# Kernel tuning notes

Hardware: AMD Instinct MI355X
Metric: run time of the kernel (lower is better)

Reference implementation:

```python
import jax, jax.numpy as jnp
import numpy as np

B, T, L, DC, DW, H, V = 128, 256, 4, 128, 128, 256, 6000
NEG = -1e30

def _lstm(x, c, h, kernel, bias):
    # TF BasicLSTMCell, forget_bias=0, gate order i, j, f, o
    z = jnp.concatenate([x, h], axis=-1) @ kernel + bias
    i, j, f, o = jnp.split(z, 4, axis=-1)
    nc = c * jax.nn.sigmoid(f) + jax.nn.sigmoid(i) * jnp.tanh(j)
    nh = jnp.tanh(nc) * jax.nn.sigmoid(o)
    return nc, nh

def _forward(chars, char_emb, reset_W, reset_b, com_W, com_b, lstm_kernel, lstm_bias, pred_W, pred_b, score_U, bos):
    Bn, Tn = chars.shape
    dt = char_emb.dtype
    # init agenda entry: BoS vector through LSTM from zero state
    c0 = jnp.zeros((Bn, H), dt)
    h0 = jnp.zeros((Bn, H), dt)
    x0 = jnp.broadcast_to(bos, (Bn, DW))
    c1, h1 = _lstm(x0, c0, h0, lstm_kernel, lstm_bias)
    pred0 = jnp.tanh(h1 @ pred_W + pred_b)
    # rolling buffer over the last L agenda entries (slot w-1 = position t-w)
    buf_pred = jnp.repeat(pred0[:, None, :], L, axis=1)
    buf_c = jnp.repeat(c1[:, None, :], L, axis=1)
    buf_h = jnp.repeat(h1[:, None, :], L, axis=1)
    # windows[t, b, j] = char at position t-j (age j), front-padded
    padded = jnp.pad(chars, ((0, 0), (L - 1, 0)))
    gi = jnp.arange(Tn)[:, None] + (L - 1) - jnp.arange(L)[None, :]
    windows = jnp.transpose(padded[:, gi], (1, 0, 2))  # [T, B, L]
    wlens = jnp.arange(1, L + 1)
    cmask = (jnp.arange(L)[None, :] < wlens[:, None]).astype(dt)  # [W, C]
    inv_len = (1.0 / wlens).astype(dt)

    def step(carry, xs):
        buf_pred, buf_c, buf_h = carry
        window, t = xs
        emb = char_emb[window]  # [B, L, DC] (ages 0..L-1)
        # per-wlen reset gate (separate weights per word length)
        g = jax.nn.sigmoid(jnp.einsum('bcd,wde->bwce', emb, reset_W) + reset_b[None, :, None, :])
        proj = jnp.tanh(jnp.einsum('bwcd,de->bwce', g * emb[:, None], com_W) + com_b)  # [B,W,C,DW]
        word = jnp.einsum('bwce,wc->bwe', proj, cmask) * inv_len[None, :, None]  # [B,W,DW] mean over the wlen chars
        score = jnp.sum((buf_pred + score_U) * word, axis=-1)  # [B,W] local score vs prev prediction
        score = jnp.where((wlens <= t + 1)[None, :], score, NEG)
        best = jnp.argmax(score, axis=1)  # greedy choice of word length
        b3 = best[:, None, None]
        word_b = jnp.take_along_axis(word, b3, axis=1)[:, 0]
        c_prev = jnp.take_along_axis(buf_c, b3, axis=1)[:, 0]
        h_prev = jnp.take_along_axis(buf_h, b3, axis=1)[:, 0]
        nc, nh = _lstm(word_b, c_prev, h_prev, lstm_kernel, lstm_bias)
        npred = jnp.tanh(nh @ pred_W + pred_b)
        carry = (jnp.concatenate([npred[:, None], buf_pred[:, :-1]], axis=1),
                 jnp.concatenate([nc[:, None], buf_c[:, :-1]], axis=1),
                 jnp.concatenate([nh[:, None], buf_h[:, :-1]], axis=1))
        best_score = jnp.take_along_axis(score, best[:, None], axis=1)[:, 0]
        return carry, (best_score, best + 1)

    _, (scores, wl) = jax.lax.scan(step, (buf_pred, buf_c, buf_h), (windows, jnp.arange(Tn)))
    return scores.T, wl.T  # [B,T] best local score, [B,T] chosen word length

def setup_inputs() -> dict:
    key = jax.random.key(0)
    ks = jax.random.split(key, 12)
    f = lambda k, s: 0.1 * jax.random.normal(k, s, dtype=jnp.float32)
    return {
        'chars': jax.random.randint(ks[0], (B, T), 0, V, dtype=jnp.int32),
        'char_emb': f(ks[1], (V, DC)),
        'reset_W': f(ks[2], (L, DC, DC)),
        'reset_b': f(ks[3], (L, DC)),
        'com_W': f(ks[4], (DC, DW)),
        'com_b': f(ks[5], (DW,)),
        'lstm_kernel': f(ks[6], (DW + H, 4 * H)),
        'lstm_bias': jnp.zeros((4 * H,), jnp.float32),
        'pred_W': f(ks[7], (H, DW)),
        'pred_b': f(ks[8], (DW,)),
        'score_U': f(ks[9], (DW,)),
        'bos': f(ks[10], (DW,)),
    }

def reference(chars, char_emb, reset_W, reset_b, com_W, com_b, lstm_kernel, lstm_bias, pred_W, pred_b, score_U, bos):
    return _forward(chars, char_emb, reset_W, reset_b, com_W, com_b, lstm_kernel, lstm_bias, pred_W, pred_b, score_U, bos)
```

## Files before the change

### kernel.cpp

```cpp
#include <hip/hip_runtime.h>

#define B_ 128
#define T_ 256
#define L_ 4
#define DC_ 128
#define DW_ 128
#define H_ 256
#define V_ 6000
#define Z4_ 1024
#define S_ 4
#define R_ 2
#define G_ 64
#define NEGF -1e30f

#define WS_VTAB  4096
#define WS_NH    (WS_VTAB + V_*L_*DW_*4)
#define WS_PP    (WS_NH + (size_t)2*G_*R_*H_*8)

typedef unsigned long long u64w;

__device__ __forceinline__ float sigm(float x) { return 1.0f / (1.0f + expf(-x)); }
__device__ __forceinline__ void pub64(u64w* p, float v, unsigned stamp) {
  u64w w = ((u64w)__float_as_uint(v) << 32) | (u64w)stamp;
  __hip_atomic_store(p, w, __ATOMIC_RELAXED, __HIP_MEMORY_SCOPE_AGENT);
}
__device__ __forceinline__ u64w ld64(const u64w* p) {
  return __hip_atomic_load(p, __ATOMIC_RELAXED, __HIP_MEMORY_SCOPE_AGENT);
}
__device__ __forceinline__ float hi32(u64w w) {
  return __uint_as_float((unsigned)(w >> 32));
}
__device__ __forceinline__ float bcast(float v, int l) {
  return __int_as_float(__builtin_amdgcn_readlane(__float_as_int(v), l));
}
__device__ __forceinline__ int amax4(const float* sc) {
  float bs = sc[0]; int bw = 0;
  if (sc[1] > bs) { bs = sc[1]; bw = 1; }
  if (sc[2] > bs) { bs = sc[2]; bw = 2; }
  if (sc[3] > bs) { bs = sc[3]; bw = 3; }
  return bw;
}
__device__ __forceinline__ float invlen(int w) {
  return (w == 0) ? 1.0f : (w == 1) ? 0.5f : (w == 2) ? (1.0f / 3.0f) : 0.25f;
}

__global__ __launch_bounds__(512) void vtab_kernel(
    const float* __restrict__ char_emb, const float* __restrict__ reset_W,
    const float* __restrict__ reset_b, const float* __restrict__ com_W,
    const float* __restrict__ com_b, float* __restrict__ Vtab)
{
  const int v = blockIdx.x;
  const int tid = threadIdx.x;
  const int w = tid >> 7;
  const int e = tid & 127;
  __shared__ float emb[DC_];
  __shared__ float ge[L_][DC_];
  if (tid < DC_) emb[tid] = char_emb[v * DC_ + tid];
  __syncthreads();
  float acc = reset_b[w * DC_ + e];
  const float* W = reset_W + (size_t)w * DC_ * DC_;
  #pragma unroll 8
  for (int k = 0; k < DC_; ++k) acc = fmaf(emb[k], W[k * DC_ + e], acc);
  ge[w][e] = sigm(acc) * emb[e];
  __syncthreads();
  float acc2 = com_b[e];
  #pragma unroll 8
  for (int k = 0; k < DC_; ++k) acc2 = fmaf(ge[w][k], com_W[k * DW_ + e], acc2);
  Vtab[((size_t)v * L_ + w) * DW_ + e] = tanhf(acc2);
}

__global__ __launch_bounds__(512, 2) void seq_kernel(
    const int* __restrict__ chars, const float* __restrict__ Vtab,
    const float* __restrict__ Kmat, const float* __restrict__ lstm_bias,
    const float* __restrict__ pred_W, const float* __restrict__ pred_b,
    const float* __restrict__ score_U, const float* __restrict__ bos,
    float* __restrict__ out, u64w* __restrict__ nh_mb, u64w* __restrict__ pp_mb)
{
  const int blk = blockIdx.x;
  const int s = blk >> 6;
  const int g = blk & 63;
  const int tid = threadIdx.x;
  const int lane = tid & 63;
  const int wv = tid >> 6;
  const int c = tid & 255;
  const int koff = (tid < 256) ? 0 : 192;
  const int colg = (c >> 6) * H_ + s * 64 + (c & 63);
  const int row0 = g * R_;

  float wreg[192];
  #pragma unroll
  for (int i = 0; i < 192; ++i)
    wreg[i] = Kmat[(size_t)(koff + i) * Z4_ + colg];

  __shared__ float ringVt[R_][4][512];
  __shared__ float pring[4][R_][DW_];
  __shared__ float zring[4][R_][256];
  __shared__ float cring[4][R_][64];
  __shared__ float zhA[R_][256];
  __shared__ float zhB[R_][256];
  __shared__ float zxL[R_][256];
  __shared__ float predWL[64][128];
  __shared__ float h1tmp[H_];
  __shared__ int   charsL[R_][T_];
  __shared__ float biasC[256], UL[128], pbL[128];
  __shared__ float scL[R_][L_];

  if (tid < 256) biasC[tid] = lstm_bias[(tid >> 6) * H_ + s * 64 + (tid & 63)];
  if (tid < 128) { UL[tid] = score_U[tid]; pbL[tid] = pred_b[tid]; }
  for (int i = tid; i < 64 * 128; i += 512)
    predWL[i >> 7][i & 127] = pred_W[(size_t)(s * 64 + (i >> 7)) * DW_ + (i & 127)];
  for (int i = tid; i < R_ * T_; i += 512)
    charsL[i >> 8][i & 255] = chars[(row0 + (i >> 8)) * T_ + (i & 255)];
  for (int i = tid; i < R_ * 4 * 512; i += 512) ((float*)ringVt)[i] = 0.0f;
  __syncthreads();

  {
    float* zb = &zring[0][0][0];
    for (int c2 = tid; c2 < Z4_; c2 += 512) {
      float a = lstm_bias[c2];
      #pragma unroll 8
      for (int k = 0; k < DC_; ++k) a = fmaf(bos[k], Kmat[(size_t)k * Z4_ + c2], a);
      zb[c2] = a;
    }
    __syncthreads();
    if (tid < H_) {
      float zi = zb[tid], zj = zb[H_ + tid], zo = zb[3 * H_ + tid];
      float nc = sigm(zi) * tanhf(zj);
      float nh = tanhf(nc) * sigm(zo);
      h1tmp[tid] = nh;
      int hl = tid - s * 64;
      if (hl >= 0 && hl < 64) {
        #pragma unroll
        for (int q = 0; q < 4; ++q)
          #pragma unroll
          for (int r = 0; r < R_; ++r) cring[q][r][hl] = nc;
      }
    }
    __syncthreads();
    {
      int kq = tid >> 7, e = tid & 127;
      float a = 0.0f;
      #pragma unroll 8
      for (int k = kq * 64; k < kq * 64 + 64; ++k)
        a = fmaf(h1tmp[k], pred_W[(size_t)k * DW_ + e], a);
      ((float*)zhA)[kq * 128 + e] = a;
    }
    __syncthreads();
    if (tid < 128) {
      const float* pa = (const float*)zhA;
      float p = tanhf(pbL[tid] + pa[tid] + pa[128 + tid] + pa[256 + tid] + pa[384 + tid]);
      #pragma unroll
      for (int q = 0; q < 4; ++q)
        #pragma unroll
        for (int r = 0; r < R_; ++r) pring[q][r][tid] = p;
    }
    __syncthreads();
    {
      float a = 0.0f;
      if (tid < 256) {
        #pragma unroll
        for (int k = 0; k < 64; ++k) a = fmaf(h1tmp[k], wreg[128 + k], a);
      } else {
        #pragma unroll
        for (int k = 0; k < 192; ++k) a = fmaf(h1tmp[64 + k], wreg[k], a);
      }
      __syncthreads();
      if (tid < 256) zhA[0][c] = a; else zhB[0][c] = a;
    }
    __syncthreads();
    if (tid < 256) {
      float z1 = zhA[0][tid] + zhB[0][tid];
      #pragma unroll
      for (int q = 0; q < 4; ++q)
        #pragma unroll
        for (int r = 0; r < R_; ++r) zring[q][r][tid] = z1;
    }
    __syncthreads();
  }

  for (int t = 0; t < T_; ++t) {
    const int slot = t & 3;
    const int parR = (t - 1) & 1;
    const int parW = t & 1;
    const unsigned stR = (unsigned)t;
    const unsigned stW = (unsigned)(t + 1);

    if ((wv >> 1) == 1) {
      int i2 = tid & 127;
      #pragma unroll
      for (int r = 0; r < R_; ++r) {
        const float* vp = Vtab + (size_t)charsL[r][t] * 512;
        #pragma unroll
        for (int q = 0; q < 4; ++q) ringVt[r][slot][q * 128 + i2] = vp[q * 128 + i2];
      }
    }

    if (t > 0) {
      const u64w* nb = nh_mb + ((size_t)parR * G_ + g) * (R_ * H_);
      if (wv < 2) {
        const u64w* ppb = pp_mb + ((size_t)parR * G_ + g) * (S_ * R_ * 128) + wv * 128;
        u64w pw0[S_], pw1[S_], nw0, nw1;
        for (;;) {
          #pragma unroll
          for (int sp = 0; sp < S_; ++sp) {
            pw0[sp] = ld64(ppb + (size_t)sp * (R_ * 128) + lane);
            pw1[sp] = ld64(ppb + (size_t)sp * (R_ * 128) + lane + 64);
          }
          nw0 = ld64(nb + lane);
          nw1 = ld64(nb + H_ + lane);
          int ok = ((unsigned)nw0 == stR) & ((unsigned)nw1 == stR);
          #pragma unroll
          for (int sp = 0; sp < S_; ++sp)
            ok &= ((unsigned)pw0[sp] == stR) & ((unsigned)pw1[sp] == stR);
          if (__all(ok)) break;
          __builtin_amdgcn_s_sleep(1);
        }
        float a0 = pbL[lane], a1 = pbL[lane + 64];
        #pragma unroll
        for (int sp = 0; sp < S_; ++sp) {
          a0 += hi32(pw0[sp]);
          a1 += hi32(pw1[sp]);
        }
        int ps = (t - 1) & 3;
        pring[ps][wv][lane] = tanhf(a0);
        pring[ps][wv][lane + 64] = tanhf(a1);
        float nv0 = hi32(nw0), nv1 = hi32(nw1);
        float z0 = 0.0f, z1 = 0.0f;
        #pragma unroll
        for (int k = 0; k < 64; ++k) {
          float w = wreg[128 + k];
          z0 = fmaf(bcast(nv0, k), w, z0);
          z1 = fmaf(bcast(nv1, k), w, z1);
        }
        zhA[0][c] = z0; zhA[1][c] = z1;
      } else if (wv < 4) {
        u64w nw0, nw1;
        for (;;) {
          nw0 = ld64(nb + lane);
          nw1 = ld64(nb + H_ + lane);
          int ok = ((unsigned)nw0 == stR) & ((unsigned)nw1 == stR);
          if (__all(ok)) break;
          __builtin_amdgcn_s_sleep(1);
        }
        float nv0 = hi32(nw0), nv1 = hi32(nw1);
        float z0 = 0.0f, z1 = 0.0f;
        #pragma unroll
        for (int k = 0; k < 64; ++k) {
          float w = wreg[128 + k];
          z0 = fmaf(bcast(nv0, k), w, z0);
          z1 = fmaf(bcast(nv1, k), w, z1);
        }
        zhA[0][c] = z0; zhA[1][c] = z1;
      } else {
        u64w nw[2][3];
        for (;;) {
          #pragma unroll
          for (int r = 0; r < 2; ++r)
            #pragma unroll
            for (int j = 0; j < 3; ++j)
              nw[r][j] = ld64(nb + (size_t)r * H_ + 64 + j * 64 + lane);
          int ok = 1;
          #pragma unroll
          for (int r = 0; r < 2; ++r)
            #pragma unroll
            for (int j = 0; j < 3; ++j)
              ok &= ((unsigned)nw[r][j] == stR);
          if (__all(ok)) break;
          __builtin_amdgcn_s_sleep(1);
        }
        float a0 = 0.0f, a1 = 0.0f;
        #pragma unroll
        for (int j = 0; j < 3; ++j) {
          float nv0 = hi32(nw[0][j]), nv1 = hi32(nw[1][j]);
          #pragma unroll
          for (int k = 0; k < 64; ++k) {
            float w = wreg[j * 64 + k];
            a0 = fmaf(bcast(nv0, k), w, a0);
            a1 = fmaf(bcast(nv1, k), w, a1);
          }
        }
        zhB[0][c] = a0; zhB[1][c] = a1;
      }
    }
    __syncthreads();

    if (t > 0) {
      int r = tid >> 8, cc = tid & 255;
      zring[(t - 1) & 3][r][cc] = zhA[r][cc] + zhB[r][cc];
    }
    {
      int r = wv >> 2, w = wv & 3;
      int ps = (t - 1 - w) & 3;
      float il = invlen(w);
      float acc = 0.0f;
      #pragma unroll
      for (int hf = 0; hf < 2; ++hf) {
        int e = lane + hf * 64;
        float sa = 0.0f;
        #pragma unroll
        for (int c2 = 0; c2 < L_; ++c2)
          if (c2 <= w) sa += ringVt[r][(t - c2) & 3][w * 128 + e];
        acc = fmaf(pring[ps][r][e] + UL[e], sa * il, acc);
      }
      #pragma unroll
      for (int off = 32; off; off >>= 1) acc += __shfl_down(acc, off);
      if (lane == 0) scL[r][w] = (w <= t) ? acc : NEGF;
    }
    __syncthreads();

    if (tid < 256) {
      float vt0[2], vt1[2];
      #pragma unroll
      for (int r = 0; r < 2; ++r) {
        int bw = amax4(scL[r]);
        float il = invlen(bw);
        float v0 = 0.f, v1 = 0.f;
        #pragma unroll
        for (int c2 = 0; c2 < L_; ++c2)
          if (c2 <= bw) {
            v0 += ringVt[r][(t - c2) & 3][bw * 128 + lane];
            v1 += ringVt[r][(t - c2) & 3][bw * 128 + 64 + lane];
          }
        vt0[r] = v0 * il; vt1[r] = v1 * il;
      }
      float a0 = 0.f, a1 = 0.f;
      #pragma unroll
      for (int k = 0; k < 64; ++k) {
        float w0 = wreg[k], w1 = wreg[64 + k];
        a0 = fmaf(bcast(vt0[0], k), w0, a0);
        a1 = fmaf(bcast(vt0[1], k), w0, a1);
        a0 = fmaf(bcast(vt1[0], k), w1, a0);
        a1 = fmaf(bcast(vt1[1], k), w1, a1);
      }
      zxL[0][c] = a0; zxL[1][c] = a1;
      if (s == 0 && tid < R_) {
        int bw = amax4(scL[tid]);
        out[(row0 + tid) * T_ + t] = scL[tid][bw];
        out[B_ * T_ + (row0 + tid) * T_ + t] = (float)(bw + 1);
      }
    }
    __syncthreads();

    if (tid < 128) {
      int r = wv, hl = lane;
      int bw = amax4(scL[r]);
      int zs = (t - 1 - bw) & 3;
      float zg[4];
      #pragma unroll
      for (int gi = 0; gi < 4; ++gi) {
        int cc = gi * 64 + hl;
        zg[gi] = biasC[cc] + zring[zs][r][cc] + zxL[r][cc];
      }
      float cp = cring[zs][r][hl];
      float nc = cp * sigm(zg[2]) + sigm(zg[0]) * tanhf(zg[1]);
      float nh = tanhf(nc) * sigm(zg[3]);
      cring[slot][r][hl] = nc;
      pub64(&nh_mb[((size_t)parW * G_ + g) * (R_ * H_) + (size_t)r * H_ + s * 64 + hl],
            nh, stW);
      float p0 = 0.f, p1 = 0.f;
      #pragma unroll
      for (int kk = 0; kk < 64; ++kk) {
        float nb2 = __shfl(nh, kk, 64);
        p0 = fmaf(nb2, predWL[kk][lane], p0);
        p1 = fmaf(nb2, predWL[kk][lane + 64], p1);
      }
      u64w* pb = pp_mb + ((size_t)parW * G_ + g) * (S_ * R_ * 128)
               + (size_t)s * (R_ * 128) + (size_t)r * 128;
      pub64(pb + lane, p0, stW);
      pub64(pb + lane + 64, p1, stW);
    }
  }
}

extern "C" void kernel_launch(void* const* d_in, const int* in_sizes, int n_in,
                              void* d_out, int out_size, void* d_ws, size_t ws_size,
                              hipStream_t stream) {
  const int*   chars     = (const int*)d_in[0];
  const float* char_emb  = (const float*)d_in[1];
  const float* reset_W   = (const float*)d_in[2];
  const float* reset_b   = (const float*)d_in[3];
  const float* com_W     = (const float*)d_in[4];
  const float* com_b     = (const float*)d_in[5];
  const float* lstm_k    = (const float*)d_in[6];
  const float* lstm_bias = (const float*)d_in[7];
  const float* pred_W    = (const float*)d_in[8];
  const float* pred_b    = (const float*)d_in[9];
  const float* score_U   = (const float*)d_in[10];
  const float* bos       = (const float*)d_in[11];

  char* ws = (char*)d_ws;
  float* Vtab = (float*)(ws + WS_VTAB);
  u64w* nh_mb = (u64w*)(ws + WS_NH);
  u64w* pp_mb = (u64w*)(ws + WS_PP);

  vtab_kernel<<<V_, 512, 0, stream>>>(char_emb, reset_W, reset_b, com_W, com_b, Vtab);
  seq_kernel<<<256, 512, 0, stream>>>(chars, Vtab, lstm_k, lstm_bias, pred_W,
                                      pred_b, score_U, bos, (float*)d_out,
                                      nh_mb, pp_mb);
}
```

Before: 2.275 ms.

## Rebalance per-step work across waves and raise priority on critical path

Restructures the per-timestep schedule. Waves 0-3 now compute the word scores for both rows, then their 64-wide recurrent h-projection. Waves 4-7 split their 192-wide h-projection, running one third in the score phase and the remaining two thirds alongside the zx projection, and write zring directly, which removes the zhB buffer and one combine pass. It also raises wave priority (s_setprio) around the prediction reduction and the LSTM/publish section that other blocks wait on, and replaces __shfl with bcast. The aim is to balance work across waves and shorten the cross-block critical path, at the cost of more register pressure from the held mailbox values.

```diff
diff --git a/kernel.cpp b/kernel.cpp
--- a/kernel.cpp
+++ b/kernel.cpp
@@ -97,7 +97,6 @@
   __shared__ float zring[4][R_][256];
   __shared__ float cring[4][R_][64];
   __shared__ float zhA[R_][256];
-  __shared__ float zhB[R_][256];
   __shared__ float zxL[R_][256];
   __shared__ float predWL[64][128];
   __shared__ float h1tmp[H_];
@@ -165,11 +164,11 @@
         for (int k = 0; k < 192; ++k) a = fmaf(h1tmp[64 + k], wreg[k], a);
       }
       __syncthreads();
-      if (tid < 256) zhA[0][c] = a; else zhB[0][c] = a;
+      if (tid < 256) ((float*)zhA)[c] = a; else ((float*)zhA)[256 + c] = a;
     }
     __syncthreads();
     if (tid < 256) {
-      float z1 = zhA[0][tid] + zhB[0][tid];
+      float z1 = ((float*)zhA)[tid] + ((float*)zhA)[256 + tid];
       #pragma unroll
       for (int q = 0; q < 4; ++q)
         #pragma unroll
@@ -184,6 +183,11 @@
     const int parW = t & 1;
     const unsigned stR = (unsigned)t;
     const unsigned stW = (unsigned)(t + 1);
+    const u64w* nb = nh_mb + ((size_t)parR * G_ + g) * (R_ * H_);
+
+    u64w nwreg0, nwreg1;
+    u64w nwU[2][3];
+    float zh0 = 0.0f, zh1 = 0.0f;
 
     if ((wv >> 1) == 1) {
       int i2 = tid & 127;
@@ -196,7 +200,6 @@
     }
 
     if (t > 0) {
-      const u64w* nb = nh_mb + ((size_t)parR * G_ + g) * (R_ * H_);
       if (wv < 2) {
         const u64w* ppb = pp_mb + ((size_t)parR * G_ + g) * (S_ * R_ * 128) + wv * 128;
         u64w pw0[S_], pw1[S_], nw0, nw1;
@@ -215,6 +218,7 @@
           if (__all(ok)) break;
           __builtin_amdgcn_s_sleep(1);
         }
+        __builtin_amdgcn_s_setprio(1);
         float a0 = pbL[lane], a1 = pbL[lane + 64];
         #pragma unroll
         for (int sp = 0; sp < S_; ++sp) {
@@ -224,15 +228,8 @@
         int ps = (t - 1) & 3;
         pring[ps][wv][lane] = tanhf(a0);
         pring[ps][wv][lane + 64] = tanhf(a1);
-        float nv0 = hi32(nw0), nv1 = hi32(nw1);
-        float z0 = 0.0f, z1 = 0.0f;
-        #pragma unroll
-        for (int k = 0; k < 64; ++k) {
-          float w = wreg[128 + k];
-          z0 = fmaf(bcast(nv0, k), w, z0);
-          z1 = fmaf(bcast(nv1, k), w, z1);
-        }
-        zhA[0][c] = z0; zhA[1][c] = z1;
+        __builtin_amdgcn_s_setprio(0);
+        nwreg0 = nw0; nwreg1 = nw1;
       } else if (wv < 4) {
         u64w nw0, nw1;
         for (;;) {
@@ -242,69 +239,66 @@
           if (__all(ok)) break;
           __builtin_amdgcn_s_sleep(1);
         }
-        float nv0 = hi32(nw0), nv1 = hi32(nw1);
-        float z0 = 0.0f, z1 = 0.0f;
-        #pragma unroll
-        for (int k = 0; k < 64; ++k) {
-          float w = wreg[128 + k];
-          z0 = fmaf(bcast(nv0, k), w, z0);
-          z1 = fmaf(bcast(nv1, k), w, z1);
-        }
-        zhA[0][c] = z0; zhA[1][c] = z1;
+        nwreg0 = nw0; nwreg1 = nw1;
       } else {
-        u64w nw[2][3];
         for (;;) {
           #pragma unroll
           for (int r = 0; r < 2; ++r)
             #pragma unroll
             for (int j = 0; j < 3; ++j)
-              nw[r][j] = ld64(nb + (size_t)r * H_ + 64 + j * 64 + lane);
+              nwU[r][j] = ld64(nb + (size_t)r * H_ + 64 + j * 64 + lane);
           int ok = 1;
           #pragma unroll
           for (int r = 0; r < 2; ++r)
             #pragma unroll
             for (int j = 0; j < 3; ++j)
-              ok &= ((unsigned)nw[r][j] == stR);
+              ok &= ((unsigned)nwU[r][j] == stR);
           if (__all(ok)) break;
           __builtin_amdgcn_s_sleep(1);
         }
+      }
+    }
+    __syncthreads();
+
+    if (wv < 4) {
+      #pragma unroll
+      for (int r = 0; r < 2; ++r) {
+        int w = wv;
+        int ps = (t - 1 - w) & 3;
+        float il = invlen(w);
+        float acc = 0.0f;
+        #pragma unroll
+        for (int hf = 0; hf < 2; ++hf) {
+          int e = lane + hf * 64;
+          float sa = 0.0f;
+          #pragma unroll
+          for (int c2 = 0; c2 < L_; ++c2)
+            if (c2 <= w) sa += ringVt[r][(t - c2) & 3][w * 128 + e];
+          acc = fmaf(pring[ps][r][e] + UL[e], sa * il, acc);
+        }
+        #pragma unroll
+        for (int off = 32; off; off >>= 1) acc += __shfl_down(acc, off);
+        if (lane == 0) scL[r][w] = (w <= t) ? acc : NEGF;
+      }
+      if (t > 0) {
+        float nv0 = hi32(nwreg0), nv1 = hi32(nwreg1);
         float a0 = 0.0f, a1 = 0.0f;
         #pragma unroll
-        for (int j = 0; j < 3; ++j) {
-          float nv0 = hi32(nw[0][j]), nv1 = hi32(nw[1][j]);
-          #pragma unroll
-          for (int k = 0; k < 64; ++k) {
-            float w = wreg[j * 64 + k];
-            a0 = fmaf(bcast(nv0, k), w, a0);
-            a1 = fmaf(bcast(nv1, k), w, a1);
-          }
-        }
-        zhB[0][c] = a0; zhB[1][c] = a1;
-      }
-    }
-    __syncthreads();
-
-    if (t > 0) {
-      int r = tid >> 8, cc = tid & 255;
-      zring[(t - 1) & 3][r][cc] = zhA[r][cc] + zhB[r][cc];
-    }
-    {
-      int r = wv >> 2, w = wv & 3;
-      int ps = (t - 1 - w) & 3;
-      float il = invlen(w);
-      float acc = 0.0f;
-      #pragma unroll
-      for (int hf = 0; hf < 2; ++hf) {
-        int e = lane + hf * 64;
-        float sa = 0.0f;
-        #pragma unroll
-        for (int c2 = 0; c2 < L_; ++c2)
-          if (c2 <= w) sa += ringVt[r][(t - c2) & 3][w * 128 + e];
-        acc = fmaf(pring[ps][r][e] + UL[e], sa * il, acc);
-      }
-      #pragma unroll
-      for (int off = 32; off; off >>= 1) acc += __shfl_down(acc, off);
-      if (lane == 0) scL[r][w] = (w <= t) ? acc : NEGF;
+        for (int k = 0; k < 64; ++k) {
+          float w = wreg[128 + k];
+          a0 = fmaf(bcast(nv0, k), w, a0);
+          a1 = fmaf(bcast(nv1, k), w, a1);
+        }
+        zhA[0][c] = a0; zhA[1][c] = a1;
+      }
+    } else if (t > 0) {
+      float nv0 = hi32(nwU[0][0]), nv1 = hi32(nwU[1][0]);
+      #pragma unroll
+      for (int k = 0; k < 64; ++k) {
+        float w = wreg[k];
+        zh0 = fmaf(bcast(nv0, k), w, zh0);
+        zh1 = fmaf(bcast(nv1, k), w, zh1);
+      }
     }
     __syncthreads();
 
@@ -338,10 +332,25 @@
         out[(row0 + tid) * T_ + t] = scL[tid][bw];
         out[B_ * T_ + (row0 + tid) * T_ + t] = (float)(bw + 1);
       }
+    } else if (t > 0) {
+      #pragma unroll
+      for (int j = 1; j < 3; ++j) {
+        float nv0 = hi32(nwU[0][j]), nv1 = hi32(nwU[1][j]);
+        #pragma unroll
+        for (int k = 0; k < 64; ++k) {
+          float w = wreg[j * 64 + k];
+          zh0 = fmaf(bcast(nv0, k), w, zh0);
+          zh1 = fmaf(bcast(nv1, k), w, zh1);
+        }
+      }
+      int zs2 = (t - 1) & 3;
+      zring[zs2][0][c] = zhA[0][c] + zh0;
+      zring[zs2][1][c] = zhA[1][c] + zh1;
     }
     __syncthreads();
 
     if (tid < 128) {
+      __builtin_amdgcn_s_setprio(1);
       int r = wv, hl = lane;
       int bw = amax4(scL[r]);
       int zs = (t - 1 - bw) & 3;
@@ -360,7 +369,7 @@
       float p0 = 0.f, p1 = 0.f;
       #pragma unroll
       for (int kk = 0; kk < 64; ++kk) {
-        float nb2 = __shfl(nh, kk, 64);
+        float nb2 = bcast(nh, kk);
         p0 = fmaf(nb2, predWL[kk][lane], p0);
         p1 = fmaf(nb2, predWL[kk][lane + 64], p1);
       }
@@ -368,6 +377,7 @@
                + (size_t)s * (R_ * 128) + (size_t)r * 128;
       pub64(pb + lane, p0, stW);
       pub64(pb + lane + 64, p1, stW);
+      __builtin_amdgcn_s_setprio(0);
     }
   }
 }
```

Result: slower. 6.471 ms (+184.4%).
